# Kernel tuning notes

Measured on AMD Instinct MI355X. Metric: run time of the kernel, lower is better.

Reference implementation:

```python
import jax, jax.numpy as jnp
import numpy as np

VOCAB = 100000
DIM = 128
B = 16384
K = 10


def setup_inputs() -> dict:
    key = jax.random.key(0)
    k1, k2, k3, k4, k5 = jax.random.split(key, 5)
    initrange = 0.5 / DIM
    return {
        "center_id": jax.random.randint(k1, (B,), 0, VOCAB),
        "pos_context_id": jax.random.randint(k2, (B,), 0, VOCAB),
        "neg_context_ids": jax.random.randint(k3, (B, K), 0, VOCAB),
        "W_in": jax.random.uniform(k4, (VOCAB, DIM), jnp.float32, -initrange, initrange),
        "W_out": jax.random.uniform(k5, (VOCAB, DIM), jnp.float32, -initrange, initrange),
    }


def reference(center_id, pos_context_id, neg_context_ids, W_in, W_out):
    center = W_in[center_id]            # [B, D]
    pos = W_out[pos_context_id]         # [B, D]
    neg = W_out[neg_context_ids]        # [B, K, D]
    pos_score = jnp.sum(center * pos, axis=1)              # [B]
    pos_loss = jax.nn.log_sigmoid(pos_score)               # [B]
    neg_score = jnp.einsum("bkd,bd->bk", neg, center)      # [B, K]
    neg_score = jnp.sum(neg_score, axis=1)                 # [B] (sum over negatives first, as in original)
    neg_loss = jax.nn.log_sigmoid(-neg_score)              # [B]
    loss = jnp.sum(pos_loss) + jnp.sum(neg_loss)
    return -loss
```

## Files before the change

### kernel.cpp

```cpp
#include <hip/hip_runtime.h>
#include <math.h>

constexpr int VOCAB = 100000;
constexpr int DIM   = 128;
constexpr int B     = 16384;
constexpr int K     = 10;
constexpr int BPB   = 8;
constexpr int GRID  = B / BPB;

__global__ __launch_bounds__(256) void skipgram_partial_kernel(
    const int*   __restrict__ center_id,
    const int*   __restrict__ pos_id,
    const int*   __restrict__ neg_ids,
    const float* __restrict__ W_in,
    const float* __restrict__ W_out,
    float*       __restrict__ partial)
{
    const int tid    = threadIdx.x;
    const int lane32 = tid & 31;
    const int sub    = tid >> 5;
    const int b      = blockIdx.x * BPB + sub;

    const int cid = center_id[b];
    const int pid = pos_id[b];
    int nid[K];
#pragma unroll
    for (int k = 0; k < K; ++k) nid[k] = neg_ids[b * K + k];

    const float4 c = ((const float4*)(W_in  + (size_t)cid * DIM))[lane32];
    const float4 p = ((const float4*)(W_out + (size_t)pid * DIM))[lane32];

    float4 ns = make_float4(0.f, 0.f, 0.f, 0.f);
#pragma unroll
    for (int k = 0; k < K; ++k) {
        const float4 n = ((const float4*)(W_out + (size_t)nid[k] * DIM))[lane32];
        ns.x += n.x; ns.y += n.y; ns.z += n.z; ns.w += n.w;
    }

    float pos_partial = c.x * p.x  + c.y * p.y  + c.z * p.z  + c.w * p.w;
    float neg_partial = c.x * ns.x + c.y * ns.y + c.z * ns.z + c.w * ns.w;

#pragma unroll
    for (int m = 16; m >= 1; m >>= 1) {
        pos_partial += __shfl_xor(pos_partial, m, 64);
        neg_partial += __shfl_xor(neg_partial, m, 64);
    }

    __shared__ float blocksum[BPB];
    if (lane32 == 0) {
        const float ps  = pos_partial;
        const float nsc = neg_partial;
        const float lp = fminf(ps,   0.f) - log1pf(expf(-fabsf(ps)));
        const float ln = fminf(-nsc, 0.f) - log1pf(expf(-fabsf(nsc)));
        blocksum[sub] = lp + ln;
    }
    __syncthreads();

    if (tid == 0) {
        float s = 0.f;
#pragma unroll
        for (int i = 0; i < BPB; ++i) s += blocksum[i];
        partial[blockIdx.x] = s;
    }
}

__global__ __launch_bounds__(256) void skipgram_reduce_kernel(
    const float* __restrict__ partial,
    float*       __restrict__ out)
{
    const int tid = threadIdx.x;
    const float4* p4 = (const float4*)partial;

    float s = 0.f;
#pragma unroll
    for (int i = 0; i < 2; ++i) {
        const float4 v = p4[tid + i * 256];
        s += v.x + v.y + v.z + v.w;
    }

#pragma unroll
    for (int m = 32; m >= 1; m >>= 1) s += __shfl_xor(s, m, 64);

    __shared__ float wsum[4];
    if ((tid & 63) == 0) wsum[tid >> 6] = s;
    __syncthreads();

    if (tid == 0) out[0] = -(wsum[0] + wsum[1] + wsum[2] + wsum[3]);
}

extern "C" void kernel_launch(void* const* d_in, const int* in_sizes, int n_in,
                              void* d_out, int out_size, void* d_ws, size_t ws_size,
                              hipStream_t stream) {
    const int*   center_id = (const int*)  d_in[0];
    const int*   pos_id    = (const int*)  d_in[1];
    const int*   neg_ids   = (const int*)  d_in[2];
    const float* W_in      = (const float*)d_in[3];
    const float* W_out     = (const float*)d_in[4];
    float*       out       = (float*)d_out;
    float*       partial   = (float*)d_ws;

    skipgram_partial_kernel<<<GRID, 256, 0, stream>>>(
        center_id, pos_id, neg_ids, W_in, W_out, partial);
    skipgram_reduce_kernel<<<1, 256, 0, stream>>>(partial, out);
}
```

Baseline: 124.6 us.

## Fuse partial and final reduction into one cooperative kernel with grid sync

Merges the two kernels into a single cooperative launch: 1024 blocks each handle two chunks of the batch, write a per-block partial, then a grid-wide sync lets block 0 do the final reduction. This removes the second kernel launch and its gap, and halves the number of partials. In exchange it adds a grid barrier and the cooperative launch path, and it requires all 1024 blocks to be co-resident. The two sequential passes per block may also reduce the number of gathers in flight per wave.

```diff
diff --git a/kernel.cpp b/kernel.cpp
--- a/kernel.cpp
+++ b/kernel.cpp
@@ -1,91 +1,93 @@
 #include <hip/hip_runtime.h>
+#include <hip/hip_cooperative_groups.h>
 #include <math.h>
+
+namespace cg = cooperative_groups;
 
 constexpr int VOCAB = 100000;
 constexpr int DIM   = 128;
 constexpr int B     = 16384;
 constexpr int K     = 10;
 constexpr int BPB   = 8;
-constexpr int GRID  = B / BPB;
+constexpr int GRID  = 1024;
+constexpr int CHUNK = GRID * BPB;
 
-__global__ __launch_bounds__(256) void skipgram_partial_kernel(
+__global__ __launch_bounds__(256, 4) void skipgram_fused_kernel(
     const int*   __restrict__ center_id,
     const int*   __restrict__ pos_id,
     const int*   __restrict__ neg_ids,
     const float* __restrict__ W_in,
     const float* __restrict__ W_out,
-    float*       __restrict__ partial)
+    float*       __restrict__ partial,
+    float*       __restrict__ out)
 {
     const int tid    = threadIdx.x;
     const int lane32 = tid & 31;
     const int sub    = tid >> 5;
-    const int b      = blockIdx.x * BPB + sub;
 
-    const int cid = center_id[b];
-    const int pid = pos_id[b];
-    int nid[K];
-#pragma unroll
-    for (int k = 0; k < K; ++k) nid[k] = neg_ids[b * K + k];
-
-    const float4 c = ((const float4*)(W_in  + (size_t)cid * DIM))[lane32];
-    const float4 p = ((const float4*)(W_out + (size_t)pid * DIM))[lane32];
-
-    float4 ns = make_float4(0.f, 0.f, 0.f, 0.f);
-#pragma unroll
-    for (int k = 0; k < K; ++k) {
-        const float4 n = ((const float4*)(W_out + (size_t)nid[k] * DIM))[lane32];
-        ns.x += n.x; ns.y += n.y; ns.z += n.z; ns.w += n.w;
-    }
-
-    float pos_partial = c.x * p.x  + c.y * p.y  + c.z * p.z  + c.w * p.w;
-    float neg_partial = c.x * ns.x + c.y * ns.y + c.z * ns.z + c.w * ns.w;
+    float acc = 0.f;
 
 #pragma unroll
-    for (int m = 16; m >= 1; m >>= 1) {
-        pos_partial += __shfl_xor(pos_partial, m, 64);
-        neg_partial += __shfl_xor(neg_partial, m, 64);
+    for (int pass = 0; pass < 2; ++pass) {
+        const int b = pass * CHUNK + blockIdx.x * BPB + sub;
+
+        const int cid = center_id[b];
+        const int pid = pos_id[b];
+        int nid[K];
+#pragma unroll
+        for (int k = 0; k < K; ++k) nid[k] = neg_ids[b * K + k];
+
+        const float4 c = ((const float4*)(W_in  + (size_t)cid * DIM))[lane32];
+        const float4 p = ((const float4*)(W_out + (size_t)pid * DIM))[lane32];
+
+        float4 ns = make_float4(0.f, 0.f, 0.f, 0.f);
+#pragma unroll
+        for (int k = 0; k < K; ++k) {
+            const float4 n = ((const float4*)(W_out + (size_t)nid[k] * DIM))[lane32];
+            ns.x += n.x; ns.y += n.y; ns.z += n.z; ns.w += n.w;
+        }
+
+        float pos_partial = c.x * p.x  + c.y * p.y  + c.z * p.z  + c.w * p.w;
+        float neg_partial = c.x * ns.x + c.y * ns.y + c.z * ns.z + c.w * ns.w;
+
+#pragma unroll
+        for (int m = 16; m >= 1; m >>= 1) {
+            pos_partial += __shfl_xor(pos_partial, m, 64);
+            neg_partial += __shfl_xor(neg_partial, m, 64);
+        }
+
+        if (lane32 == 0) {
+            const float ps  = pos_partial;
+            const float nsc = neg_partial;
+            const float lp = fminf(ps,   0.f) - log1pf(expf(-fabsf(ps)));
+            const float ln = fminf(-nsc, 0.f) - log1pf(expf(-fabsf(nsc)));
+            acc += lp + ln;
+        }
     }
 
     __shared__ float blocksum[BPB];
-    if (lane32 == 0) {
-        const float ps  = pos_partial;
-        const float nsc = neg_partial;
-        const float lp = fminf(ps,   0.f) - log1pf(expf(-fabsf(ps)));
-        const float ln = fminf(-nsc, 0.f) - log1pf(expf(-fabsf(nsc)));
-        blocksum[sub] = lp + ln;
-    }
+    if (lane32 == 0) blocksum[sub] = acc;
     __syncthreads();
-
     if (tid == 0) {
         float s = 0.f;
 #pragma unroll
         for (int i = 0; i < BPB; ++i) s += blocksum[i];
         partial[blockIdx.x] = s;
     }
-}
 
-__global__ __launch_bounds__(256) void skipgram_reduce_kernel(
-    const float* __restrict__ partial,
-    float*       __restrict__ out)
-{
-    const int tid = threadIdx.x;
-    const float4* p4 = (const float4*)partial;
+    cg::this_grid().sync();
 
-    float s = 0.f;
+    if (blockIdx.x == 0) {
+        const float4 v = ((const float4*)partial)[tid];
+        float s = v.x + v.y + v.z + v.w;
 #pragma unroll
-    for (int i = 0; i < 2; ++i) {
-        const float4 v = p4[tid + i * 256];
-        s += v.x + v.y + v.z + v.w;
+        for (int m = 32; m >= 1; m >>= 1) s += __shfl_xor(s, m, 64);
+
+        __shared__ float wsum[4];
+        if ((tid & 63) == 0) wsum[tid >> 6] = s;
+        __syncthreads();
+        if (tid == 0) out[0] = -(wsum[0] + wsum[1] + wsum[2] + wsum[3]);
     }
-
-#pragma unroll
-    for (int m = 32; m >= 1; m >>= 1) s += __shfl_xor(s, m, 64);
-
-    __shared__ float wsum[4];
-    if ((tid & 63) == 0) wsum[tid >> 6] = s;
-    __syncthreads();
-
-    if (tid == 0) out[0] = -(wsum[0] + wsum[1] + wsum[2] + wsum[3]);
 }
 
 extern "C" void kernel_launch(void* const* d_in, const int* in_sizes, int n_in,
@@ -99,7 +101,10 @@
     float*       out       = (float*)d_out;
     float*       partial   = (float*)d_ws;
 
-    skipgram_partial_kernel<<<GRID, 256, 0, stream>>>(
-        center_id, pos_id, neg_ids, W_in, W_out, partial);
-    skipgram_reduce_kernel<<<1, 256, 0, stream>>>(partial, out);
+    void* args[] = {
+        (void*)&center_id, (void*)&pos_id, (void*)&neg_ids,
+        (void*)&W_in, (void*)&W_out, (void*)&partial, (void*)&out
+    };
+    hipLaunchCooperativeKernel((const void*)skipgram_fused_kernel,
+                               dim3(GRID), dim3(256), args, 0, stream);
 }
```

Measured after the change: 243.7 us. +95.5%, slower.
